# Optimization experiments

Measured on AMD Instinct MI355X. Metric: run time of the kernel, lower is better.

The kernel has to match this reference:

```python
import jax, jax.numpy as jnp
import numpy as np

B, T, D = 32, 4096, 256
P, K, L = 2, 17, 3
NH, HD, FF, HID = 8, 32, 2048, 128


def _ln(x, w, b):
    m = x.mean(-1, keepdims=True)
    v = ((x - m) ** 2).mean(-1, keepdims=True)
    return (x - m) * jax.lax.rsqrt(v + 1e-5) * w + b


def _refine(x, w1, b1, w2, b2):
    # x: (B,P,K,D). Vectorized all-pairs: pair[b,p,i,j] = concat(x_i, x_j); MLP; mean over j; residual.
    xi = jnp.broadcast_to(x[:, :, :, None, :], (B, P, K, K, D))
    xj = jnp.broadcast_to(x[:, :, None, :, :], (B, P, K, K, D))
    pair = jnp.concatenate([xi, xj], axis=-1)  # (B,P,K,K,2D)
    h = jax.nn.relu(pair @ w1.T + b1)
    y = (h @ w2.T + b2).mean(axis=3)  # (B,P,K,D)
    return y + x


def _forward(memory, person_q, key_q, sa_in_w, sa_in_b, sa_out_w, sa_out_b,
             ca_in_w, ca_in_b, ca_out_w, ca_out_b, ff1_w, ff1_b, ff2_w, ff2_b,
             ln1_w, ln1_b, ln2_w, ln2_b, ln3_w, ln3_b,
             r1_w1, r1_b1, r1_w2, r1_b2, r2_w1, r2_b1, r2_w2, r2_b2, fc_w, fc_b):
    scale = 1.0 / np.sqrt(HD).astype(np.float32)
    # tgt for person p = person_q[p] + key_q, all persons vectorized into axis P
    x = jnp.broadcast_to(person_q[None, :, None, :] + key_q[None, None, :, :], (B, P, K, D))
    for l in range(L):
        # --- self-attention over K keypoint queries (post-norm TransformerDecoderLayer) ---
        qkv = x @ sa_in_w[l].T + sa_in_b[l]
        q, k, v = jnp.split(qkv, 3, axis=-1)
        qh = q.reshape(B, P, K, NH, HD)
        kh = k.reshape(B, P, K, NH, HD)
        vh = v.reshape(B, P, K, NH, HD)
        a = jax.nn.softmax(jnp.einsum('bpqhd,bpkhd->bphqk', qh, kh) * scale, axis=-1)
        o = jnp.einsum('bphqk,bpkhd->bpqhd', a, vh).reshape(B, P, K, D)
        x = _ln(x + o @ sa_out_w[l].T + sa_out_b[l], ln1_w[l], ln1_b[l])
        # --- cross-attention to memory; memory K/V computed once, shared across persons ---
        q = x @ ca_in_w[l][:D].T + ca_in_b[l][:D]
        mk = memory @ ca_in_w[l][D:2 * D].T + ca_in_b[l][D:2 * D]
        mv = memory @ ca_in_w[l][2 * D:].T + ca_in_b[l][2 * D:]
        qh = q.reshape(B, P, K, NH, HD)
        kh = mk.reshape(B, T, NH, HD)
        vh = mv.reshape(B, T, NH, HD)
        a = jax.nn.softmax(jnp.einsum('bpqhd,bthd->bphqt', qh, kh) * scale, axis=-1)
        o = jnp.einsum('bphqt,bthd->bpqhd', a, vh).reshape(B, P, K, D)
        x = _ln(x + o @ ca_out_w[l].T + ca_out_b[l], ln2_w[l], ln2_b[l])
        # --- feed-forward (ReLU, dim_feedforward=2048 default) ---
        h = jax.nn.relu(x @ ff1_w[l].T + ff1_b[l])
        x = _ln(x + h @ ff2_w[l].T + ff2_b[l], ln3_w[l], ln3_b[l])
    x = _refine(x, r1_w1, r1_b1, r1_w2, r1_b2)
    x = _refine(x, r2_w1, r2_b1, r2_w2, r2_b2)
    return x @ fc_w.T + fc_b  # (B, P, K, 3)


def setup_inputs() -> dict:
    key = jax.random.key(0)
    ks = iter(jax.random.split(key, 48))

    def w(shape, s=0.02):
        return jax.random.normal(next(ks), shape, dtype=jnp.float32) * s

    inp = {
        'memory': jax.random.normal(next(ks), (B, T, D), dtype=jnp.float32),
        'person_q': jax.random.normal(next(ks), (P, D), dtype=jnp.float32),
        'key_q': jax.random.normal(next(ks), (K, D), dtype=jnp.float32),
        'sa_in_w': w((L, 3 * D, D)), 'sa_in_b': jnp.zeros((L, 3 * D)),
        'sa_out_w': w((L, D, D)), 'sa_out_b': jnp.zeros((L, D)),
        'ca_in_w': w((L, 3 * D, D)), 'ca_in_b': jnp.zeros((L, 3 * D)),
        'ca_out_w': w((L, D, D)), 'ca_out_b': jnp.zeros((L, D)),
        'ff1_w': w((L, FF, D)), 'ff1_b': jnp.zeros((L, FF)),
        'ff2_w': w((L, D, FF)), 'ff2_b': jnp.zeros((L, D)),
        'ln1_w': jnp.ones((L, D)), 'ln1_b': jnp.zeros((L, D)),
        'ln2_w': jnp.ones((L, D)), 'ln2_b': jnp.zeros((L, D)),
        'ln3_w': jnp.ones((L, D)), 'ln3_b': jnp.zeros((L, D)),
        'r1_w1': w((HID, 2 * D)), 'r1_b1': jnp.zeros((HID,)),
        'r1_w2': w((D, HID)), 'r1_b2': jnp.zeros((D,)),
        'r2_w1': w((HID, 2 * D)), 'r2_b1': jnp.zeros((HID,)),
        'r2_w2': w((D, HID)), 'r2_b2': jnp.zeros((D,)),
        'fc_w': w((3, D)), 'fc_b': jnp.zeros((3,)),
    }
    return inp


def reference(memory, person_q, key_q, sa_in_w, sa_in_b, sa_out_w, sa_out_b,
              ca_in_w, ca_in_b, ca_out_w, ca_out_b, ff1_w, ff1_b, ff2_w, ff2_b,
              ln1_w, ln1_b, ln2_w, ln2_b, ln3_w, ln3_b,
              r1_w1, r1_b1, r1_w2, r1_b2, r2_w1, r2_b1, r2_w2, r2_b2, fc_w, fc_b):
    return _forward(memory, person_q, key_q, sa_in_w, sa_in_b, sa_out_w, sa_out_b,
                    ca_in_w, ca_in_b, ca_out_w, ca_out_b, ff1_w, ff1_b, ff2_w, ff2_b,
                    ln1_w, ln1_b, ln2_w, ln2_b, ln3_w, ln3_b,
                    r1_w1, r1_b1, r1_w2, r1_b2, r2_w1, r2_b1, r2_w2, r2_b2, fc_w, fc_b)
```

## Files before the change

kernel.cpp:

```cpp
#include <hip/hip_runtime.h>
#include <stdint.h>

#define NB   32
#define TSEQ 4096
#define DD   256
#define PP   2
#define KK   17
#define LL   3
#define NHH  8
#define HDD  32
#define FFD  2048
#define HIDD 128
#define ROWS 1088
#define SCALE 0.17677669529663689f

typedef __attribute__((ext_vector_type(4))) float f32x4;
typedef __attribute__((ext_vector_type(8))) short bf16x8;

static __device__ __forceinline__ unsigned cvtpk(float lo, float hi) {
  unsigned r;
  asm volatile("v_cvt_pk_bf16_f32 %0, %1, %2" : "=v"(r) : "v"(lo), "v"(hi));
  return r;
}
static __device__ __forceinline__ unsigned short f2bf(float f) {
  unsigned int x = __float_as_uint(f);
  return (unsigned short)((x + 0x7fffu + ((x >> 16) & 1u)) >> 16);
}
static __device__ __forceinline__ void gload_lds16(const void* g, void* l) {
  __builtin_amdgcn_global_load_lds(
      (const __attribute__((address_space(1))) unsigned int*)g,
      (__attribute__((address_space(3))) unsigned int*)l, 16, 0, 0);
}

struct CvtJob { const float* src; unsigned short* dst; int n; };
struct CvtJobs8 { CvtJob j[8]; };
__global__ __launch_bounds__(256) void cvt_multi_kernel(CvtJobs8 jobs) {
#pragma unroll
  for (int jj = 0; jj < 8; ++jj) {
    const float* src = jobs.j[jj].src;
    unsigned short* dst = jobs.j[jj].dst;
    const int n8 = jobs.j[jj].n >> 3;
    for (int i = blockIdx.x * 256 + threadIdx.x; i < n8; i += gridDim.x * 256) {
      const float4 f0 = *reinterpret_cast<const float4*>(src + i * 8);
      const float4 f1 = *reinterpret_cast<const float4*>(src + i * 8 + 4);
      uint4 st;
      st.x = cvtpk(f0.x, f0.y); st.y = cvtpk(f0.z, f0.w);
      st.z = cvtpk(f1.x, f1.y); st.w = cvtpk(f1.z, f1.w);
      *reinterpret_cast<uint4*>(dst + i * 8) = st;
    }
  }
}

__global__ __launch_bounds__(256) void prep_small_kernel(
    const float* __restrict__ person_q, const float* __restrict__ key_q,
    const float* __restrict__ ca_in_w, const float* __restrict__ ca_in_b,
    const float* __restrict__ ca_out_w, const float* __restrict__ ca_out_b,
    float* __restrict__ x, unsigned short* __restrict__ x_bf,
    float* __restrict__ bqk, float* __restrict__ bvo) {
  const int bx = blockIdx.x, tid = threadIdx.x;
  if (bx < ROWS) {
    const int p = (bx / KK) & 1, k = bx % KK;
    const float v = person_q[p * DD + tid] + key_q[k * DD + tid];
    x[(size_t)bx * DD + tid] = v;
    x_bf[(size_t)bx * DD + tid] = f2bf(v);
  } else if (bx < ROWS + 24) {
    const int b2 = bx - ROWS;
    const int l = b2 >> 3, h = b2 & 7;
    const float* Wk = ca_in_w + (size_t)l * 196608 + (size_t)(256 + h * 32) * 256;
    const float* bq = ca_in_b + l * 768 + h * 32;
    float acc = 0.f;
#pragma unroll
    for (int j = 0; j < 32; ++j) acc += bq[j] * Wk[(size_t)j * 256 + tid];
    bqk[(size_t)l * 2048 + h * 256 + tid] = acc * SCALE;
  } else {
    const int l = bx - ROWS - 24;
    float acc = ca_out_b[l * 256 + tid];
    for (int j = 0; j < 256; ++j)
      acc += ca_out_w[(size_t)l * 65536 + (size_t)tid * 256 + j] * ca_in_b[l * 768 + 512 + j];
    bvo[l * 256 + tid] = acc;
  }
}

__global__ __launch_bounds__(256) void gemm_bf16_kernel(
    const unsigned short* __restrict__ Xbf, const unsigned short* __restrict__ Wbf,
    const float* __restrict__ bias, const float* __restrict__ R,
    float* __restrict__ Yf, unsigned short* __restrict__ Ybf,
    int M, int N, int K, int wstride, int relu) {
  __shared__ unsigned short Xs[64 * 64];
  __shared__ unsigned short Ws[64 * 64];
  const int tid = threadIdx.x, lane = tid & 63, w = tid >> 6;
  const int g = lane >> 4, q16 = lane & 15;
  const int m0 = blockIdx.y * 64, n0 = blockIdx.x * 64;
  f32x4 acc[4];
#pragma unroll
  for (int nt = 0; nt < 4; ++nt) acc[nt] = (f32x4){0.f, 0.f, 0.f, 0.f};

  for (int k0 = 0; k0 < K; k0 += 64) {
    __syncthreads();
#pragma unroll
    for (int j = 0; j < 2; ++j) {
      const int cc = w * 2 + j;
      const int row = cc * 8 + (lane >> 3);
      const int sc = (lane & 7) ^ (row & 7);
      gload_lds16(Xbf + (size_t)(m0 + row) * K + k0 + sc * 8, &Xs[cc * 512]);
      gload_lds16(Wbf + (size_t)(n0 + row) * wstride + k0 + sc * 8, &Ws[cc * 512]);
    }
    asm volatile("s_waitcnt vmcnt(0)" ::: "memory");
    __syncthreads();
    const int arow = w * 16 + q16;
#pragma unroll
    for (int ks = 0; ks < 2; ++ks) {
      const bf16x8 a = *reinterpret_cast<const bf16x8*>(
          &Xs[arow * 64 + ((((ks << 2) + g) ^ (arow & 7)) << 3)]);
#pragma unroll
      for (int nt = 0; nt < 4; ++nt) {
        const int brow = nt * 16 + q16;
        const bf16x8 bfr = *reinterpret_cast<const bf16x8*>(
            &Ws[brow * 64 + ((((ks << 2) + g) ^ (brow & 7)) << 3)]);
        acc[nt] = __builtin_amdgcn_mfma_f32_16x16x32_bf16(a, bfr, acc[nt], 0, 0, 0);
      }
    }
  }
#pragma unroll
  for (int nt = 0; nt < 4; ++nt) {
    const int n = n0 + nt * 16 + q16;
    const float bv = bias ? bias[n] : 0.f;
#pragma unroll
    for (int r = 0; r < 4; ++r) {
      const int m = m0 + w * 16 + g * 4 + r;
      float o = acc[nt][r] + bv;
      if (relu) o = fmaxf(o, 0.f);
      if (R) o += R[(size_t)m * N + n];
      if (Yf) Yf[(size_t)m * N + n] = o;
      if (Ybf) Ybf[(size_t)m * N + n] = f2bf(o);
    }
  }
}

__global__ __launch_bounds__(256) void gemm_bf16_sk_kernel(
    const unsigned short* __restrict__ Xbf, const unsigned short* __restrict__ Wbf,
    float* __restrict__ part, int M, int N, int K, int wstride, int kslice) {
  __shared__ unsigned short Xs[64 * 64];
  __shared__ unsigned short Ws[64 * 64];
  const int tid = threadIdx.x, lane = tid & 63, w = tid >> 6;
  const int g = lane >> 4, q16 = lane & 15;
  const int m0 = blockIdx.y * 64, n0 = blockIdx.x * 64;
  const int kz = blockIdx.z;
  const int kbeg = kz * kslice, kend = kbeg + kslice;
  f32x4 acc[4];
#pragma unroll
  for (int nt = 0; nt < 4; ++nt) acc[nt] = (f32x4){0.f, 0.f, 0.f, 0.f};

  for (int k0 = kbeg; k0 < kend; k0 += 64) {
    __syncthreads();
#pragma unroll
    for (int j = 0; j < 2; ++j) {
      const int cc = w * 2 + j;
      const int row = cc * 8 + (lane >> 3);
      const int sc = (lane & 7) ^ (row & 7);
      gload_lds16(Xbf + (size_t)(m0 + row) * K + k0 + sc * 8, &Xs[cc * 512]);
      gload_lds16(Wbf + (size_t)(n0 + row) * wstride + k0 + sc * 8, &Ws[cc * 512]);
    }
    asm volatile("s_waitcnt vmcnt(0)" ::: "memory");
    __syncthreads();
    const int arow = w * 16 + q16;
#pragma unroll
    for (int ks = 0; ks < 2; ++ks) {
      const bf16x8 a = *reinterpret_cast<const bf16x8*>(
          &Xs[arow * 64 + ((((ks << 2) + g) ^ (arow & 7)) << 3)]);
#pragma unroll
      for (int nt = 0; nt < 4; ++nt) {
        const int brow = nt * 16 + q16;
        const bf16x8 bfr = *reinterpret_cast<const bf16x8*>(
            &Ws[brow * 64 + ((((ks << 2) + g) ^ (brow & 7)) << 3)]);
        acc[nt] = __builtin_amdgcn_mfma_f32_16x16x32_bf16(a, bfr, acc[nt], 0, 0, 0);
      }
    }
  }
  float* pout = part + (size_t)kz * M * N;
#pragma unroll
  for (int nt = 0; nt < 4; ++nt) {
    const int n = n0 + nt * 16 + q16;
#pragma unroll
    for (int r = 0; r < 4; ++r) {
      const int m = m0 + w * 16 + g * 4 + r;
      pout[(size_t)m * N + n] = acc[nt][r];
    }
  }
}

__global__ __launch_bounds__(256) void ln_red_kernel(
    const float* __restrict__ xin, const float* __restrict__ parts, int np,
    const float* __restrict__ bias, const float* __restrict__ w,
    const float* __restrict__ b, float* __restrict__ xout,
    unsigned short* __restrict__ xout_bf) {
  const int row = blockIdx.x, tid = threadIdx.x;
  const size_t base = (size_t)row * DD + tid;
  float v = xin[base] + bias[tid];
  for (int p = 0; p < np; ++p) v += parts[(size_t)p * ROWS * DD + base];
  float s = v, s2 = v * v;
#pragma unroll
  for (int off = 32; off > 0; off >>= 1) {
    s += __shfl_down(s, off);
    s2 += __shfl_down(s2, off);
  }
  __shared__ float ps[4], ps2[4];
  if ((tid & 63) == 0) { ps[tid >> 6] = s; ps2[tid >> 6] = s2; }
  __syncthreads();
  const float st = ps[0] + ps[1] + ps[2] + ps[3];
  const float st2 = ps2[0] + ps2[1] + ps2[2] + ps2[3];
  const float mean = st * (1.f / 256.f);
  const float var = st2 * (1.f / 256.f) - mean * mean;
  const float inv = rsqrtf(var + 1e-5f);
  const float o = (v - mean) * inv * w[tid] + b[tid];
  xout[base] = o;
  xout_bf[base] = f2bf(o);
}

__global__ __launch_bounds__(256) void fc_kernel(
    const float* __restrict__ x, const float* __restrict__ fc_w,
    const float* __restrict__ fc_b, float* __restrict__ out) {
  const int row = blockIdx.x * 4 + (threadIdx.x >> 6);
  const int lane = threadIdx.x & 63;
  float xr[4];
#pragma unroll
  for (int j = 0; j < 4; ++j) xr[j] = x[(size_t)row * DD + lane + 64 * j];
#pragma unroll
  for (int o = 0; o < 3; ++o) {
    float s = 0.f;
#pragma unroll
    for (int j = 0; j < 4; ++j) s += xr[j] * fc_w[o * DD + lane + 64 * j];
#pragma unroll
    for (int off = 32; off > 0; off >>= 1) s += __shfl_down(s, off);
    if (lane == 0) out[(size_t)row * 3 + o] = s + fc_b[o];
  }
}

__global__ __launch_bounds__(64) void sa_attn_kernel(
    const float* __restrict__ qkv, unsigned short* __restrict__ attn_bf) {
  const int blk = blockIdx.x;
  const int h = blk & 7, bp = blk >> 3;
  const int rowbase = bp * KK;
  const int tid = threadIdx.x;
  __shared__ float qs[KK][36], ks[KK][36], vs[KK][36];
  __shared__ float ss[KK][20];
  __shared__ float lsum[KK];
  for (int i = tid; i < KK * HDD; i += 64) {
    const int r = i >> 5, d = i & 31;
    const size_t base = (size_t)(rowbase + r) * 768 + h * 32 + d;
    qs[r][d] = qkv[base];
    ks[r][d] = qkv[base + 256];
    vs[r][d] = qkv[base + 512];
  }
  __syncthreads();
  for (int i = tid; i < KK * KK; i += 64) {
    const int q = i / KK, k = i % KK;
    float s = 0.f;
#pragma unroll
    for (int d = 0; d < HDD; ++d) s += qs[q][d] * ks[k][d];
    ss[q][k] = s * SCALE;
  }
  __syncthreads();
  if (tid < KK) {
    float m = -1e30f;
    for (int k = 0; k < KK; ++k) m = fmaxf(m, ss[tid][k]);
    float l = 0.f;
    for (int k = 0; k < KK; ++k) { const float e = __expf(ss[tid][k] - m); ss[tid][k] = e; l += e; }
    lsum[tid] = l;
  }
  __syncthreads();
  for (int i = tid; i < KK * HDD; i += 64) {
    const int q = i >> 5, d = i & 31;
    float o = 0.f;
#pragma unroll
    for (int k = 0; k < KK; ++k) o += ss[q][k] * vs[k][d];
    attn_bf[(size_t)(rowbase + q) * DD + h * 32 + d] = f2bf(o / lsum[q]);
  }
}

__global__ __launch_bounds__(256) void wqkvo_kernel(
    const float* __restrict__ ca_in_w, const float* __restrict__ ca_out_w,
    const float* __restrict__ r1_w1, const float* __restrict__ r2_w1,
    unsigned short* __restrict__ Wqk_bf, unsigned short* __restrict__ Wvo_bf,
    unsigned short* __restrict__ rpack_bf) {
  const int bx0 = blockIdx.x;
  if (bx0 < 6144) {
    const int l = bx0 >> 11, hc = bx0 & 2047;
    const int h = hc >> 8, c = hc & 255;
    const int d = threadIdx.x;
    const float* Wq = ca_in_w + (size_t)l * 196608 + (size_t)(h * 32) * 256;
    const float* Wk = ca_in_w + (size_t)l * 196608 + (size_t)(256 + h * 32) * 256;
    float acc = 0.f;
#pragma unroll
    for (int j = 0; j < 32; ++j) acc += Wk[(size_t)j * 256 + c] * Wq[(size_t)j * 256 + d];
    Wqk_bf[((size_t)l * 2048 + hc) * 256 + d] = f2bf(acc * SCALE);
  } else if (bx0 < 12288) {
    const int bx = bx0 - 6144;
    const int h = bx & 7, dp = (bx >> 3) & 255, l = bx >> 11;
    const int c = threadIdx.x;
    const float* wout = ca_out_w + (size_t)l * 65536 + (size_t)dp * 256 + h * 32;
    const float* wv = ca_in_w + (size_t)l * 196608 + (size_t)(512 + h * 32) * 256 + c;
    float acc = 0.f;
#pragma unroll
    for (int j = 0; j < 32; ++j) acc += wout[j] * wv[(size_t)j * 256];
    Wvo_bf[((size_t)l * 256 + dp) * 2048 + h * 256 + c] = f2bf(acc);
  } else {
    const int bx2 = bx0 - 12288;
    const int rr = bx2 >> 8, n = bx2 & 255;
    const float* w1 = rr ? r2_w1 : r1_w1;
    const float v = (n < 128) ? w1[(size_t)n * 512 + threadIdx.x]
                              : w1[(size_t)(n - 128) * 512 + 256 + threadIdx.x];
    rpack_bf[(size_t)rr * 65536 + (size_t)n * 256 + threadIdx.x] = f2bf(v);
  }
}

__global__ __launch_bounds__(256) void prep_mem_kernel(
    const float* __restrict__ memory, unsigned short* __restrict__ mem_bf,
    unsigned short* __restrict__ memT) {
  const int b = blockIdx.x >> 6, tc = blockIdx.x & 63;
  const int tid = threadIdx.x;
  __shared__ unsigned short tile[64][264];
  for (int it = 0; it < 8; ++it) {
    const int idx = it * 256 + tid;
    const int t = idx >> 5, c8 = (idx & 31) << 3;
    const size_t goff = ((size_t)b * TSEQ + tc * 64 + t) * DD + c8;
    const float4 f0 = *reinterpret_cast<const float4*>(memory + goff);
    const float4 f1 = *reinterpret_cast<const float4*>(memory + goff + 4);
    uint4 st;
    st.x = cvtpk(f0.x, f0.y); st.y = cvtpk(f0.z, f0.w);
    st.z = cvtpk(f1.x, f1.y); st.w = cvtpk(f1.z, f1.w);
    *reinterpret_cast<uint4*>(&tile[t][c8]) = st;
    *reinterpret_cast<uint4*>(mem_bf + goff) = st;
  }
  __syncthreads();
  for (int it = 0; it < 8; ++it) {
    const int idx = it * 256 + tid;
    const int c = idx >> 3, t8 = (idx & 7) << 3;
    union { unsigned short v[8]; uint4 u; } pk;
#pragma unroll
    for (int j = 0; j < 8; ++j) pk.v[j] = tile[t8 + j][c];
    *reinterpret_cast<uint4*>(&memT[((size_t)b * DD + c) * TSEQ + tc * 64 + t8]) = pk.u;
  }
}

#define PS3 72
__global__ __launch_bounds__(256, 2) void ca_fused_kernel(
    const unsigned short* __restrict__ qkeff_bf, const unsigned short* __restrict__ mem_bf,
    const unsigned short* __restrict__ memT,
    float* __restrict__ o_part, float* __restrict__ m_part, float* __restrict__ l_part) {
  const int h = blockIdx.x >> 6;
  const int b = (blockIdx.x >> 1) & 31;
  const int half = blockIdx.x & 1;
  const int tid = threadIdx.x;
  const int lane = tid & 63, w = tid >> 6;
  const int g = lane >> 4, q16 = lane & 15;

  __shared__ unsigned short mem_lds[64 * 256];
  __shared__ unsigned short memT_lds[256 * 64];
  __shared__ unsigned short p_lds[48 * PS3];
  __shared__ float red_m[4 * 48];
  __shared__ float red_l[4 * 48];
  __shared__ float r_lds[48];

  bf16x8 bq[3][8];
#pragma unroll
  for (int qt = 0; qt < 3; ++qt) {
    const int ql = qt * 16 + q16;
    if (ql < 34) {
      const unsigned short* qbase = qkeff_bf + (size_t)(b * 34 + ql) * 2048 + h * 256;
#pragma unroll
      for (int ks = 0; ks < 8; ++ks)
        bq[qt][ks] = *reinterpret_cast<const bf16x8*>(qbase + ks * 32 + g * 8);
    } else {
#pragma unroll
      for (int ks = 0; ks < 8; ++ks) bq[qt][ks] = (bf16x8){0, 0, 0, 0, 0, 0, 0, 0};
    }
  }

  f32x4 ctx[3][4];
#pragma unroll
  for (int mt = 0; mt < 3; ++mt)
#pragma unroll
    for (int nt = 0; nt < 4; ++nt) ctx[mt][nt] = (f32x4){0.f, 0.f, 0.f, 0.f};
  float m_run[3] = {-1e30f, -1e30f, -1e30f};
  float l_run[3] = {0.f, 0.f, 0.f};

  const unsigned short* membb = mem_bf + (size_t)b * TSEQ * DD;
  const unsigned short* memTb = memT + (size_t)b * DD * TSEQ;

  for (int tile = 0; tile < 32; ++tile) {
    const int tbase = half * 2048 + tile * 64;
    __syncthreads();

#pragma unroll
    for (int j = 0; j < 8; ++j) {
      const int cc = w * 8 + j;
      const int trow = cc * 2 + (lane >> 5);
      const int sc = (lane & 31) ^ (trow & 7);
      gload_lds16(membb + (size_t)(tbase + trow) * DD + sc * 8, &mem_lds[cc * 512]);
    }
#pragma unroll
    for (int j = 0; j < 8; ++j) {
      const int cc = w * 8 + j;
      const int crow = cc * 8 + (lane >> 3);
      const int sc = (lane & 7) ^ (crow & 7);
      gload_lds16(memTb + (size_t)crow * TSEQ + tbase + sc * 8, &memT_lds[cc * 512]);
    }
    asm volatile("s_waitcnt vmcnt(0)" ::: "memory");
    __syncthreads();

    f32x4 sacc[3];
#pragma unroll
    for (int qt = 0; qt < 3; ++qt) sacc[qt] = (f32x4){0.f, 0.f, 0.f, 0.f};
    {
      const int arow = w * 16 + q16;
      __builtin_amdgcn_s_setprio(1);
#pragma unroll
      for (int ks = 0; ks < 8; ++ks) {
        const bf16x8 af = *reinterpret_cast<const bf16x8*>(
            &mem_lds[arow * 256 + ((((ks << 2) + g) ^ (arow & 7)) << 3)]);
#pragma unroll
        for (int qt = 0; qt < 3; ++qt)
          sacc[qt] = __builtin_amdgcn_mfma_f32_16x16x32_bf16(af, bq[qt][ks], sacc[qt], 0, 0, 0);
      }
      __builtin_amdgcn_s_setprio(0);
    }

#pragma unroll
    for (int qt = 0; qt < 3; ++qt) {
      float v = fmaxf(fmaxf(sacc[qt][0], sacc[qt][1]), fmaxf(sacc[qt][2], sacc[qt][3]));
      v = fmaxf(v, __shfl_xor(v, 16));
      v = fmaxf(v, __shfl_xor(v, 32));
      if (lane < 16) red_m[w * 48 + qt * 16 + lane] = v;
    }
    __syncthreads();

    float tmax[3];
#pragma unroll
    for (int qt = 0; qt < 3; ++qt) {
      const int q = qt * 16 + q16;
      tmax[qt] = fmaxf(fmaxf(red_m[q], red_m[48 + q]),
                       fmaxf(red_m[96 + q], red_m[144 + q]));
    }
    const float dmax = fmaxf(fmaxf(tmax[0] - m_run[0], tmax[1] - m_run[1]),
                             tmax[2] - m_run[2]);
    const bool defer = __all(dmax <= 8.0f);
    float rfac[3] = {1.f, 1.f, 1.f};
    if (!defer) {
#pragma unroll
      for (int qt = 0; qt < 3; ++qt) {
        const float mnew = fmaxf(m_run[qt], tmax[qt]);
        rfac[qt] = __expf(m_run[qt] - mnew);
        m_run[qt] = mnew;
      }
      if (w == 0 && lane < 16) {
#pragma unroll
        for (int qt = 0; qt < 3; ++qt) r_lds[qt * 16 + lane] = rfac[qt];
      }
    }

#pragma unroll
    for (int qt = 0; qt < 3; ++qt) {
      const float p0 = __expf(sacc[qt][0] - m_run[qt]);
      const float p1 = __expf(sacc[qt][1] - m_run[qt]);
      const float p2 = __expf(sacc[qt][2] - m_run[qt]);
      const float p3 = __expf(sacc[qt][3] - m_run[qt]);
      const int prow = (qt * 16 + q16) * PS3 + w * 16 + g * 4;
      *reinterpret_cast<unsigned*>(&p_lds[prow]) = cvtpk(p0, p1);
      *reinterpret_cast<unsigned*>(&p_lds[prow + 2]) = cvtpk(p2, p3);
      float ps = (p0 + p1) + (p2 + p3);
      ps += __shfl_xor(ps, 16);
      ps += __shfl_xor(ps, 32);
      if (lane < 16) red_l[w * 48 + qt * 16 + lane] = ps;
    }
    __syncthreads();

#pragma unroll
    for (int qt = 0; qt < 3; ++qt) {
      const int q = qt * 16 + q16;
      const float ssum = (red_l[q] + red_l[48 + q]) + (red_l[96 + q] + red_l[144 + q]);
      l_run[qt] = defer ? (l_run[qt] + ssum) : (l_run[qt] * rfac[qt] + ssum);
    }
    if (!defer) {
#pragma unroll
      for (int mt = 0; mt < 3; ++mt)
#pragma unroll
        for (int r = 0; r < 4; ++r) {
          const float rr = r_lds[mt * 16 + g * 4 + r];
#pragma unroll
          for (int nt = 0; nt < 4; ++nt) ctx[mt][nt][r] *= rr;
        }
    }

    bf16x8 pf[3][2];
#pragma unroll
    for (int mt = 0; mt < 3; ++mt)
#pragma unroll
      for (int ks2 = 0; ks2 < 2; ++ks2)
        pf[mt][ks2] = *reinterpret_cast<const bf16x8*>(
            &p_lds[(mt * 16 + q16) * PS3 + ks2 * 32 + g * 8]);
    __builtin_amdgcn_s_setprio(1);
#pragma unroll
    for (int nt = 0; nt < 4; ++nt) {
      const int c = w * 64 + nt * 16 + q16;
#pragma unroll
      for (int ks2 = 0; ks2 < 2; ++ks2) {
        const bf16x8 bT = *reinterpret_cast<const bf16x8*>(
            &memT_lds[c * 64 + ((((ks2 << 2) + g) ^ (c & 7)) << 3)]);
#pragma unroll
        for (int mt = 0; mt < 3; ++mt)
          ctx[mt][nt] = __builtin_amdgcn_mfma_f32_16x16x32_bf16(pf[mt][ks2], bT,
                                                                ctx[mt][nt], 0, 0, 0);
      }
    }
    __builtin_amdgcn_s_setprio(0);
  }

#pragma unroll
  for (int mt = 0; mt < 3; ++mt)
#pragma unroll
    for (int r = 0; r < 4; ++r) {
      const int q = mt * 16 + g * 4 + r;
      if (q < 34) {
        const size_t orow = (size_t)(half * ROWS + b * 34 + q) * 2048;
#pragma unroll
        for (int nt = 0; nt < 4; ++nt)
          o_part[orow + h * 256 + w * 64 + nt * 16 + q16] = ctx[mt][nt][r];
      }
    }
  if (w == 0 && lane < 16) {
#pragma unroll
    for (int qt = 0; qt < 3; ++qt) {
      const int q = qt * 16 + lane;
      if (q < 34) {
        const size_t idx = (size_t)(half * ROWS + b * 34 + q) * 8 + h;
        m_part[idx] = m_run[qt];
        l_part[idx] = l_run[qt];
      }
    }
  }
}

__global__ __launch_bounds__(256) void ca_combine_kernel(
    const float* __restrict__ o_part, const float* __restrict__ m_part,
    const float* __restrict__ l_part, unsigned short* __restrict__ ctx_bf) {
  const int row = blockIdx.x, c = threadIdx.x;
#pragma unroll
  for (int h = 0; h < NHH; ++h) {
    const float m0 = m_part[(size_t)row * 8 + h];
    const float m1 = m_part[(size_t)(ROWS + row) * 8 + h];
    const float l0 = l_part[(size_t)row * 8 + h];
    const float l1 = l_part[(size_t)(ROWS + row) * 8 + h];
    const float M = fmaxf(m0, m1);
    const float w0 = __expf(m0 - M), w1 = __expf(m1 - M);
    const float denom = l0 * w0 + l1 * w1;
    const float o0 = o_part[(size_t)row * 2048 + h * 256 + c];
    const float o1 = o_part[(size_t)(ROWS + row) * 2048 + h * 256 + c];
    ctx_bf[(size_t)row * 2048 + h * 256 + c] = f2bf((o0 * w0 + o1 * w1) / denom);
  }
}

__global__ __launch_bounds__(256) void pairmean_kernel(
    const float* __restrict__ uv, const float* __restrict__ b1,
    unsigned short* __restrict__ hbar_bf) {
  const int bp = blockIdx.x, tid = threadIdx.x;
  const int r0 = bp * KK;
  __shared__ float us[KK][132], vs[KK][132];
  __shared__ float b1s[128];
  if (tid < 128) b1s[tid] = b1[tid];
  for (int i = tid; i < KK * HIDD; i += 256) {
    const int r = i >> 7, f = i & 127;
    us[r][f] = uv[(size_t)(r0 + r) * 256 + f];
    vs[r][f] = uv[(size_t)(r0 + r) * 256 + 128 + f];
  }
  __syncthreads();
  for (int i = tid; i < KK * HIDD; i += 256) {
    const int r = i >> 7, f = i & 127;
    const float ub = us[r][f] + b1s[f];
    float s = 0.f;
#pragma unroll
    for (int j = 0; j < KK; ++j) s += fmaxf(ub + vs[j][f], 0.f);
    hbar_bf[(size_t)(r0 + r) * HIDD + f] = f2bf(s * (1.0f / 17.0f));
  }
}

static void gemm_bf(const unsigned short* X, const unsigned short* W, const float* bias,
                    const float* R, float* Yf, unsigned short* Ybf, int M, int N, int K,
                    int wstride, int relu, hipStream_t s) {
  dim3 g(N / 64, M / 64);
  gemm_bf16_kernel<<<g, 256, 0, s>>>(X, W, bias, R, Yf, Ybf, M, N, K, wstride, relu);
}
static void gemm_sk(const unsigned short* X, const unsigned short* W, float* part,
                    int M, int N, int K, int wstride, int ksplit, hipStream_t s) {
  dim3 g(N / 64, M / 64, ksplit);
  gemm_bf16_sk_kernel<<<g, 256, 0, s>>>(X, W, part, M, N, K, wstride, K / ksplit);
}

extern "C" void kernel_launch(void* const* d_in, const int* in_sizes, int n_in,
                              void* d_out, int out_size, void* d_ws, size_t ws_size,
                              hipStream_t stream) {
  const float* memory   = (const float*)d_in[0];
  const float* person_q = (const float*)d_in[1];
  const float* key_q    = (const float*)d_in[2];
  const float* sa_in_w  = (const float*)d_in[3];
  const float* sa_in_b  = (const float*)d_in[4];
  const float* sa_out_w = (const float*)d_in[5];
  const float* sa_out_b = (const float*)d_in[6];
  const float* ca_in_w  = (const float*)d_in[7];
  const float* ca_in_b  = (const float*)d_in[8];
  const float* ca_out_w = (const float*)d_in[9];
  const float* ca_out_b = (const float*)d_in[10];
  const float* ff1_w = (const float*)d_in[11];
  const float* ff1_b = (const float*)d_in[12];
  const float* ff2_w = (const float*)d_in[13];
  const float* ff2_b = (const float*)d_in[14];
  const float* ln1_w = (const float*)d_in[15];
  const float* ln1_b = (const float*)d_in[16];
  const float* ln2_w = (const float*)d_in[17];
  const float* ln2_b = (const float*)d_in[18];
  const float* ln3_w = (const float*)d_in[19];
  const float* ln3_b = (const float*)d_in[20];
  const float* r1_w1 = (const float*)d_in[21];
  const float* r1_b1 = (const float*)d_in[22];
  const float* r1_w2 = (const float*)d_in[23];
  const float* r1_b2 = (const float*)d_in[24];
  const float* r2_w1 = (const float*)d_in[25];
  const float* r2_b1 = (const float*)d_in[26];
  const float* r2_w2 = (const float*)d_in[27];
  const float* r2_b2 = (const float*)d_in[28];
  const float* fc_w  = (const float*)d_in[29];
  const float* fc_b  = (const float*)d_in[30];
  float* out = (float*)d_out;

  char* wsb = (char*)d_ws;
  size_t off = 0;
  auto alloc = [&](size_t bytes) -> char* {
    char* p = wsb + off;
    off += (bytes + 255) & ~(size_t)255;
    return p;
  };
  float* x      = (float*)alloc((size_t)ROWS * DD * 4);
  float* qkv    = (float*)alloc((size_t)ROWS * 768 * 4);
  float* parts  = (float*)alloc((size_t)4 * ROWS * DD * 4);
  float* bvo    = (float*)alloc(3 * 256 * 4);
  float* bqk    = (float*)alloc((size_t)3 * 2048 * 4);
  float* uvbuf  = (float*)alloc((size_t)ROWS * 256 * 4);
  float* o_part = (float*)alloc((size_t)2 * ROWS * 2048 * 4);
  float* m_part = (float*)alloc((size_t)2 * ROWS * 8 * 4);
  float* l_part = (float*)alloc((size_t)2 * ROWS * 8 * 4);
  unsigned short* x_bf     = (unsigned short*)alloc((size_t)ROWS * DD * 2);
  unsigned short* attn_bf  = (unsigned short*)alloc((size_t)ROWS * DD * 2);
  unsigned short* hff_bf   = (unsigned short*)alloc((size_t)ROWS * 2048 * 2);
  unsigned short* ctx_bf   = (unsigned short*)alloc((size_t)ROWS * 2048 * 2);
  unsigned short* qkeff_bf = (unsigned short*)alloc((size_t)ROWS * 2048 * 2);
  unsigned short* hbar_bf  = (unsigned short*)alloc((size_t)ROWS * HIDD * 2);
  unsigned short* mem_bf   = (unsigned short*)alloc((size_t)NB * TSEQ * DD * 2);
  unsigned short* memT     = (unsigned short*)alloc((size_t)NB * TSEQ * DD * 2);
  unsigned short* sa_in_bf  = (unsigned short*)alloc((size_t)3 * 768 * 256 * 2);
  unsigned short* sa_out_bf = (unsigned short*)alloc((size_t)3 * 256 * 256 * 2);
  unsigned short* Wqk_bf   = (unsigned short*)alloc((size_t)3 * 2048 * 256 * 2);
  unsigned short* ff1_bf   = (unsigned short*)alloc((size_t)3 * 2048 * 256 * 2);
  unsigned short* ff2_bf   = (unsigned short*)alloc((size_t)3 * 256 * 2048 * 2);
  unsigned short* Wvo_bf   = (unsigned short*)alloc((size_t)3 * 256 * 2048 * 2);
  unsigned short* rpack_bf = (unsigned short*)alloc((size_t)2 * 256 * 256 * 2);
  unsigned short* r1w2_bf  = (unsigned short*)alloc((size_t)DD * HIDD * 2);
  unsigned short* r2w2_bf  = (unsigned short*)alloc((size_t)DD * HIDD * 2);

  prep_mem_kernel<<<NB * 64, 256, 0, stream>>>(memory, mem_bf, memT);
  CvtJobs8 jobs;
  jobs.j[0] = {sa_in_w,  sa_in_bf,  3 * 768 * 256};
  jobs.j[1] = {sa_out_w, sa_out_bf, 3 * 256 * 256};
  jobs.j[2] = {ff1_w,    ff1_bf,    3 * 2048 * 256};
  jobs.j[3] = {ff2_w,    ff2_bf,    3 * 256 * 2048};
  jobs.j[4] = {r1_w2,    r1w2_bf,   DD * HIDD};
  jobs.j[5] = {r2_w2,    r2w2_bf,   DD * HIDD};
  jobs.j[6] = {r1_w2,    r1w2_bf,   0};
  jobs.j[7] = {r2_w2,    r2w2_bf,   0};
  cvt_multi_kernel<<<1024, 256, 0, stream>>>(jobs);
  wqkvo_kernel<<<12800, 256, 0, stream>>>(ca_in_w, ca_out_w, r1_w1, r2_w1,
                                          Wqk_bf, Wvo_bf, rpack_bf);
  prep_small_kernel<<<ROWS + 24 + 3, 256, 0, stream>>>(
      person_q, key_q, ca_in_w, ca_in_b, ca_out_w, ca_out_b, x, x_bf, bqk, bvo);

  for (int l = 0; l < LL; ++l) {
    gemm_bf(x_bf, sa_in_bf + (size_t)l * 768 * 256, sa_in_b + l * 768, nullptr,
            qkv, nullptr, ROWS, 768, 256, 256, 0, stream);
    sa_attn_kernel<<<512, 64, 0, stream>>>(qkv, attn_bf);
    gemm_sk(attn_bf, sa_out_bf + (size_t)l * 256 * 256, parts,
            ROWS, 256, 256, 256, 2, stream);
    ln_red_kernel<<<ROWS, 256, 0, stream>>>(x, parts, 2, sa_out_b + l * 256,
                                            ln1_w + l * 256, ln1_b + l * 256, x, x_bf);
    gemm_bf(x_bf, Wqk_bf + (size_t)l * 2048 * 256, bqk + l * 2048, nullptr,
            nullptr, qkeff_bf, ROWS, 2048, 256, 256, 0, stream);
    ca_fused_kernel<<<512, 256, 0, stream>>>(qkeff_bf, mem_bf, memT, o_part, m_part, l_part);
    ca_combine_kernel<<<ROWS, 256, 0, stream>>>(o_part, m_part, l_part, ctx_bf);
    gemm_sk(ctx_bf, Wvo_bf + (size_t)l * 256 * 2048, parts,
            ROWS, 256, 2048, 2048, 4, stream);
    ln_red_kernel<<<ROWS, 256, 0, stream>>>(x, parts, 4, bvo + l * 256,
                                            ln2_w + l * 256, ln2_b + l * 256, x, x_bf);
    gemm_bf(x_bf, ff1_bf + (size_t)l * 2048 * 256, ff1_b + l * 2048, nullptr,
            nullptr, hff_bf, ROWS, 2048, 256, 256, 1, stream);
    gemm_sk(hff_bf, ff2_bf + (size_t)l * 256 * 2048, parts,
            ROWS, 256, 2048, 2048, 4, stream);
    ln_red_kernel<<<ROWS, 256, 0, stream>>>(x, parts, 4, ff2_b + l * 256,
                                            ln3_w + l * 256, ln3_b + l * 256, x, x_bf);
  }

  const unsigned short* rw2_bf[2] = {r1w2_bf, r2w2_bf};
  const float* rb1[2] = {r1_b1, r2_b1};
  const float* rb2[2] = {r1_b2, r2_b2};
  for (int r = 0; r < 2; ++r) {
    gemm_bf(x_bf, rpack_bf + (size_t)r * 65536, nullptr, nullptr, uvbuf, nullptr,
            ROWS, 256, 256, 256, 0, stream);
    pairmean_kernel<<<64, 256, 0, stream>>>(uvbuf, rb1[r], hbar_bf);
    gemm_bf(hbar_bf, rw2_bf[r], rb2[r], x, x, x_bf,
            ROWS, 256, 128, 128, 0, stream);
  }

  fc_kernel<<<ROWS / 4, 256, 0, stream>>>(x, fc_w, fc_b, out);
}
```

Before: 640.1 us.

## Read memory tiles directly from global in cross-attention, drop LDS staging

The cross-attention kernel no longer stages the memory and transposed-memory tiles in shared memory. Each lane now loads its MFMA operands straight from global memory (or cache), which removes two barriers per tile and 64KB of LDS. Launch bounds rise from 2 to 4 blocks per CU to use the freed LDS for more occupancy. The cost is uncoalesced per-lane 16-byte global reads with no explicit prefetch, and more register pressure under the tighter launch bound.

```diff
diff --git a/kernel.cpp b/kernel.cpp
--- a/kernel.cpp
+++ b/kernel.cpp
@@ -344,7 +344,7 @@
 }
 
 #define PS3 72
-__global__ __launch_bounds__(256, 2) void ca_fused_kernel(
+__global__ __launch_bounds__(256, 4) void ca_fused_kernel(
     const unsigned short* __restrict__ qkeff_bf, const unsigned short* __restrict__ mem_bf,
     const unsigned short* __restrict__ memT,
     float* __restrict__ o_part, float* __restrict__ m_part, float* __restrict__ l_part) {
@@ -355,8 +355,6 @@
   const int lane = tid & 63, w = tid >> 6;
   const int g = lane >> 4, q16 = lane & 15;
 
-  __shared__ unsigned short mem_lds[64 * 256];
-  __shared__ unsigned short memT_lds[256 * 64];
   __shared__ unsigned short p_lds[48 * PS3];
   __shared__ float red_m[4 * 48];
   __shared__ float red_l[4 * 48];
@@ -385,40 +383,23 @@
   float m_run[3] = {-1e30f, -1e30f, -1e30f};
   float l_run[3] = {0.f, 0.f, 0.f};
 
-  const unsigned short* membb = mem_bf + (size_t)b * TSEQ * DD;
-  const unsigned short* memTb = memT + (size_t)b * DD * TSEQ;
+  const unsigned short* amem = mem_bf + ((size_t)b * TSEQ + (size_t)(w * 16 + q16)) * DD
+                               + (size_t)half * 2048 * DD + g * 8;
+  const unsigned short* bmemT0 = memT + (size_t)b * DD * TSEQ + (size_t)half * 2048
+                                 + g * 8;
 
   for (int tile = 0; tile < 32; ++tile) {
-    const int tbase = half * 2048 + tile * 64;
-    __syncthreads();
-
-#pragma unroll
-    for (int j = 0; j < 8; ++j) {
-      const int cc = w * 8 + j;
-      const int trow = cc * 2 + (lane >> 5);
-      const int sc = (lane & 31) ^ (trow & 7);
-      gload_lds16(membb + (size_t)(tbase + trow) * DD + sc * 8, &mem_lds[cc * 512]);
-    }
-#pragma unroll
-    for (int j = 0; j < 8; ++j) {
-      const int cc = w * 8 + j;
-      const int crow = cc * 8 + (lane >> 3);
-      const int sc = (lane & 7) ^ (crow & 7);
-      gload_lds16(memTb + (size_t)crow * TSEQ + tbase + sc * 8, &memT_lds[cc * 512]);
-    }
-    asm volatile("s_waitcnt vmcnt(0)" ::: "memory");
-    __syncthreads();
+    const int t64 = tile * 64;
 
     f32x4 sacc[3];
 #pragma unroll
     for (int qt = 0; qt < 3; ++qt) sacc[qt] = (f32x4){0.f, 0.f, 0.f, 0.f};
     {
-      const int arow = w * 16 + q16;
+      const unsigned short* ap = amem + (size_t)t64 * DD;
       __builtin_amdgcn_s_setprio(1);
 #pragma unroll
       for (int ks = 0; ks < 8; ++ks) {
-        const bf16x8 af = *reinterpret_cast<const bf16x8*>(
-            &mem_lds[arow * 256 + ((((ks << 2) + g) ^ (arow & 7)) << 3)]);
+        const bf16x8 af = *reinterpret_cast<const bf16x8*>(ap + ks * 32);
 #pragma unroll
         for (int qt = 0; qt < 3; ++qt)
           sacc[qt] = __builtin_amdgcn_mfma_f32_16x16x32_bf16(af, bq[qt][ks], sacc[qt], 0, 0, 0);
@@ -503,10 +484,10 @@
 #pragma unroll
     for (int nt = 0; nt < 4; ++nt) {
       const int c = w * 64 + nt * 16 + q16;
+      const unsigned short* bp = bmemT0 + (size_t)c * TSEQ + t64;
 #pragma unroll
       for (int ks2 = 0; ks2 < 2; ++ks2) {
-        const bf16x8 bT = *reinterpret_cast<const bf16x8*>(
-            &memT_lds[c * 64 + ((((ks2 << 2) + g) ^ (c & 7)) << 3)]);
+        const bf16x8 bT = *reinterpret_cast<const bf16x8*>(bp + ks2 * 32);
 #pragma unroll
         for (int mt = 0; mt < 3; ++mt)
           ctx[mt][nt] = __builtin_amdgcn_mfma_f32_16x16x32_bf16(pf[mt][ks2], bT,
```

New measurement: 1.317 ms. 106% more time.

## Prefetch next memory tile into LDS while computing current tile in cross-attention

Applied to the files above, without the earlier changes.

The cross-attention loop now issues the global-to-LDS loads for the next 64-row tile of memory and memory-transposed data right after the current tile's reads of each buffer finish. It waits with partial vmcnt counts instead of a full drain and a barrier at the top of each tile. Each wave only loads and reads its own LDS rows, which is what allows dropping the per-tile __syncthreads. The other barriers become a bare s_barrier plus lgkmcnt waits. This hides global load latency behind the MFMA and softmax work, at the cost of relying on careful vmcnt accounting with single-buffered LDS.

```diff
diff --git a/kernel.cpp b/kernel.cpp
--- a/kernel.cpp
+++ b/kernel.cpp
@@ -376,6 +376,7 @@
       for (int ks = 0; ks < 8; ++ks) bq[qt][ks] = (bf16x8){0, 0, 0, 0, 0, 0, 0, 0};
     }
   }
+  asm volatile("s_waitcnt vmcnt(0)" ::: "memory");
 
   f32x4 ctx[3][4];
 #pragma unroll
@@ -388,10 +389,7 @@
   const unsigned short* membb = mem_bf + (size_t)b * TSEQ * DD;
   const unsigned short* memTb = memT + (size_t)b * DD * TSEQ;
 
-  for (int tile = 0; tile < 32; ++tile) {
-    const int tbase = half * 2048 + tile * 64;
-    __syncthreads();
-
+  auto stage_mem = [&](int tbase) {
 #pragma unroll
     for (int j = 0; j < 8; ++j) {
       const int cc = w * 8 + j;
@@ -399,6 +397,8 @@
       const int sc = (lane & 31) ^ (trow & 7);
       gload_lds16(membb + (size_t)(tbase + trow) * DD + sc * 8, &mem_lds[cc * 512]);
     }
+  };
+  auto stage_memT = [&](int tbase) {
 #pragma unroll
     for (int j = 0; j < 8; ++j) {
       const int cc = w * 8 + j;
@@ -406,8 +406,18 @@
       const int sc = (lane & 7) ^ (crow & 7);
       gload_lds16(memTb + (size_t)crow * TSEQ + tbase + sc * 8, &memT_lds[cc * 512]);
     }
-    asm volatile("s_waitcnt vmcnt(0)" ::: "memory");
-    __syncthreads();
+  };
+
+  const int tb0 = half * 2048;
+  stage_mem(tb0);
+  stage_memT(tb0);
+
+  for (int tile = 0; tile < 32; ++tile) {
+    const bool last = (tile == 31);
+    const int tbase_n = tb0 + (tile + 1) * 64;
+
+    asm volatile("s_waitcnt vmcnt(8)" ::: "memory");
+    asm volatile("" ::: "memory");
 
     f32x4 sacc[3];
 #pragma unroll
@@ -424,6 +434,10 @@
           sacc[qt] = __builtin_amdgcn_mfma_f32_16x16x32_bf16(af, bq[qt][ks], sacc[qt], 0, 0, 0);
       }
       __builtin_amdgcn_s_setprio(0);
+    }
+    if (!last) {
+      asm volatile("s_waitcnt lgkmcnt(0)" ::: "memory");
+      stage_mem(tbase_n);
     }
 
 #pragma unroll
@@ -433,7 +447,9 @@
       v = fmaxf(v, __shfl_xor(v, 32));
       if (lane < 16) red_m[w * 48 + qt * 16 + lane] = v;
     }
-    __syncthreads();
+    asm volatile("s_waitcnt lgkmcnt(0)" ::: "memory");
+    __builtin_amdgcn_s_barrier();
+    asm volatile("" ::: "memory");
 
     float tmax[3];
 #pragma unroll
@@ -473,7 +489,9 @@
       ps += __shfl_xor(ps, 32);
       if (lane < 16) red_l[w * 48 + qt * 16 + lane] = ps;
     }
-    __syncthreads();
+    asm volatile("s_waitcnt lgkmcnt(0)" ::: "memory");
+    __builtin_amdgcn_s_barrier();
+    asm volatile("" ::: "memory");
 
 #pragma unroll
     for (int qt = 0; qt < 3; ++qt) {
@@ -492,6 +510,13 @@
         }
     }
 
+    if (last) {
+      asm volatile("s_waitcnt vmcnt(0)" ::: "memory");
+    } else {
+      asm volatile("s_waitcnt vmcnt(8)" ::: "memory");
+    }
+    asm volatile("" ::: "memory");
+
     bf16x8 pf[3][2];
 #pragma unroll
     for (int mt = 0; mt < 3; ++mt)
@@ -514,6 +539,11 @@
       }
     }
     __builtin_amdgcn_s_setprio(0);
+
+    if (!last) {
+      asm volatile("s_waitcnt lgkmcnt(0)" ::: "memory");
+      stage_memT(tbase_n);
+    }
   }
 
 #pragma unroll
```

New measurement: 658.2 us. 2.8% more time.
